# Kernel optimization log

Hardware: AMD Instinct MI355X
Metric: run time of the kernel (lower is better)

## Reference

```python
import jax, jax.numpy as jnp
import numpy as np

B, C_IN, FH, TW = 64, 8, 128, 128
FBINS, A, M_ARR, M_SRC = 257, 360, 4, 2
EPS = 1e-6


def _conv2d(x, w):
    return jax.lax.conv_general_dilated(x, w, (1, 1), 'SAME', dimension_numbers=('NCHW', 'OIHW', 'NCHW'))


def _bn(x, g, b, m, v):
    sh = (1, -1, 1, 1)
    return (x - m.reshape(sh)) * jax.lax.rsqrt(v.reshape(sh) + 1e-5) * g.reshape(sh) + b.reshape(sh)


def _pool2(x):
    b_, c, h, w = x.shape
    return x.reshape(b_, c, h // 2, 2, w // 2, 2).max(axis=(3, 5))


def _block(x, w, g, b, m, v):
    return _pool2(jax.nn.relu(_bn(_conv2d(x, w), g, b, m, v)))


def _conv1d(x, w, b):
    return jax.lax.conv_general_dilated(x, w, (1,), 'SAME', dimension_numbers=('NCH', 'OIH', 'NCH')) + b[None, :, None]


def setup_inputs() -> dict:
    ks = jax.random.split(jax.random.key(0), 16)
    r = lambda i, shp, s=1.0: jax.random.normal(ks[i], shp, dtype=jnp.float32) * s
    d = {
        'X': r(0, (B, C_IN, FH, TW)),
        'sv_real': r(1, (B, FBINS, A, M_ARR)),
        'sv_imag': r(2, (B, FBINS, A, M_ARR)),
        'correlation': jnp.zeros((1,), jnp.float32),
        'conv1_w': r(3, (64, C_IN, 3, 3), 0.1),
        'conv2_w': r(4, (64, 64, 3, 3), 0.04),
        'conv3_w': r(5, (64, 64, 3, 3), 0.04),
        'conv4_w': r(6, (FBINS, 64, 3, 3), 0.04),
        'fc_w': r(7, (32, 64), 0.1),
        'fc_b': jnp.zeros((32,), jnp.float32),
        'convs2_w': r(8, (FBINS, FBINS, 3), 0.02),
        'convs2_b': jnp.zeros((FBINS,), jnp.float32),
        'convs1_w': r(9, (1, FBINS, 3), 0.03),
        'convs1_b': jnp.zeros((1,), jnp.float32),
        'ca_w1': r(10, (16, FBINS), 0.06),
        'ca_w2': r(11, (FBINS, 16), 0.2),
    }
    for i, c in [(1, 64), (2, 64), (3, 64), (4, FBINS)]:
        d[f'bn{i}_g'] = jnp.ones((c,), jnp.float32)
        d[f'bn{i}_b'] = jnp.zeros((c,), jnp.float32)
        d[f'bn{i}_m'] = jnp.zeros((c,), jnp.float32)
        d[f'bn{i}_v'] = jnp.ones((c,), jnp.float32)
    return d


def reference(X, sv_real, sv_imag, correlation,
              conv1_w, bn1_g, bn1_b, bn1_m, bn1_v,
              conv2_w, bn2_g, bn2_b, bn2_m, bn2_v,
              conv3_w, bn3_g, bn3_b, bn3_m, bn3_v,
              conv4_w, bn4_g, bn4_b, bn4_m, bn4_v,
              fc_w, fc_b, convs2_w, convs2_b, convs1_w, convs1_b,
              ca_w1, ca_w2):
    b_ = X.shape[0]
    # CNN encoder: (B,8,128,128) -> (B,257,8,8)
    z = _block(X, conv1_w, bn1_g, bn1_b, bn1_m, bn1_v)
    z = _block(z, conv2_w, bn2_g, bn2_b, bn2_m, bn2_v)
    z = _block(z, conv3_w, bn3_g, bn3_b, bn3_m, bn3_v)
    z = _block(z, conv4_w, bn4_g, bn4_b, bn4_m, bn4_v)
    z = z.reshape(b_, FBINS, -1) @ fc_w.T + fc_b            # (B,257,32)
    z = z.reshape(b_, FBINS, C_IN // 2, C_IN)               # (B,257,4,8)
    Rz = jax.lax.complex(z[..., :M_ARR], z[..., M_ARR:])    # (B,257,4,4)
    # hermitianize + diagonal loading
    Rz = 0.5 * (Rz + jnp.conj(jnp.swapaxes(Rz, -1, -2)))
    Rz = Rz + 1e-5 * jnp.eye(M_ARR, dtype=Rz.dtype)
    _, evecs = jnp.linalg.eigh(Rz)                          # ascending eigenvalues
    Un = evecs[..., ::-1][..., M_SRC:]                      # noise subspace (B,F,4,2)
    UnUnH = Un @ jnp.conj(jnp.swapaxes(Un, -1, -2))         # (B,F,4,4)
    svc = jnp.conj(jax.lax.complex(sv_real, sv_imag))       # (B,F,A,4)
    # faithful to torch code: denom[a] = sum_{m,n} conj(sv[a,m]) UnUnH[m,n] conj(sv[a,n])
    denom = jnp.real(jnp.einsum('bfam,bfmn,bfan->bfa', svc, UnUnH, svc))
    spectrum = 1.0 / jnp.maximum(denom, EPS)                # (B,257,360)
    spectrum = jax.nn.leaky_relu(_conv1d(spectrum, convs2_w, convs2_b), 0.1)
    # channel attention over the 257 freq channels
    y = spectrum.mean(-1)                                   # (B,257)
    att = jax.nn.sigmoid(jax.nn.relu(y @ ca_w1.T) @ ca_w2.T)
    spectrum = spectrum * att[:, :, None]
    spectrum = jax.nn.sigmoid(_conv1d(spectrum, convs1_w, convs1_b))[:, 0, :]  # (B,360)
    # soft-argmax over top-5 peaks
    angles = jnp.linspace(0.0, 360.0, A + 1)[:-1]
    vals, idx = jax.lax.top_k(spectrum, 5)
    wts = jax.nn.softmax(20.0 * vals, axis=-1)
    doa = (wts * angles[idx]).sum(-1)[:, None]              # (B,1)
    return doa, spectrum
```

## Files before the change

kernel.cpp:

```cpp
#include <hip/hip_runtime.h>

typedef unsigned short u16;
typedef unsigned int u32;
typedef short short8 __attribute__((ext_vector_type(8)));
typedef float f32x4 __attribute__((ext_vector_type(4)));

#define NB 64
#define NFB 257
#define NANG 360

template<int V> struct IC { static constexpr int value = V; };

__device__ __forceinline__ u16 f2bf(float x) {
    u32 u = __float_as_uint(x);
    u = (u + 0x7fffu + ((u >> 16) & 1u)) >> 16;
    return (u16)u;
}
__device__ __forceinline__ float bf2f(u16 h) { return __uint_as_float(((u32)h) << 16); }


__global__ __launch_bounds__(256) void bnprep(
    const float* g1, const float* b1, const float* m1, const float* v1,
    const float* g2, const float* b2, const float* m2, const float* v2,
    const float* g3, const float* b3, const float* m3, const float* v3,
    const float* g4, const float* b4, const float* m4, const float* v4,
    float* out)
{
    int L = blockIdx.x;
    const float* gs[4] = {g1, g2, g3, g4};
    const float* bs[4] = {b1, b2, b3, b4};
    const float* ms[4] = {m1, m2, m3, m4};
    const float* vs[4] = {v1, v2, v3, v4};
    int n = (L == 3) ? 257 : 64;
    float* sc = out + L * 1024;
    float* bi = sc + 512;
    for (int i = threadIdx.x; i < n; i += 256) {
        float s = gs[L][i] * rsqrtf(vs[L][i] + 1e-5f);
        sc[i] = s;
        bi[i] = bs[L][i] - ms[L][i] * s;
    }
}

__global__ __launch_bounds__(256) void bpack(
    const float* __restrict__ w, u16* __restrict__ Bp,
    int CREAL, int OCREAL, int NT, int KCC, int NFTOT)
{
    int i = blockIdx.x * 256 + threadIdx.x;
    int total = NT * KCC * 2 * NFTOT * 64;
    if (i >= total) return;
    int lane = i & 63;
    int t = i >> 6;
    int nf = t % NFTOT;
    int th = t / NFTOT;
    int h = th & 1;
    int chunk = th >> 1;
    int s = chunk / KCC, kc = chunk % KCC;
    int n = nf * 16 + (lane & 15);
    int k0 = kc * 32 + (lane >> 4) * 8;
    u16 o8[8];
    #pragma unroll
    for (int e = 0; e < 8; ++e) {
        int k = k0 + e;
        float v = 0.f;
        if (k < CREAL && n < OCREAL) v = w[((size_t)n * CREAL + k) * NT + s];
        u16 hh = f2bf(v);
        o8[e] = (h == 0) ? hh : f2bf(v - bf2f(hh));
    }
    u16* d = Bp + (size_t)i * 8;
    #pragma unroll
    for (int e = 0; e < 8; ++e) d[e] = o8[e];
}

__global__ __launch_bounds__(256) void bpack1(const float* __restrict__ w, u16* __restrict__ Bp)
{
    int i = blockIdx.x * 256 + threadIdx.x;
    if (i >= 3 * 2 * 4 * 64) return;
    int lane = i & 63;
    int t = i >> 6;
    int nf = t % 4;
    int th = t / 4;
    int h = th & 1;
    int ky = th >> 1;
    int n = nf * 16 + (lane & 15);
    int q = lane >> 4;
    u16 o8[8];
    #pragma unroll
    for (int e = 0; e < 8; ++e) {
        float v = (q < 3) ? w[((size_t)(n * 8 + e) * 3 + ky) * 3 + q] : 0.f;
        u16 hh = f2bf(v);
        o8[e] = (h == 0) ? hh : f2bf(v - bf2f(hh));
    }
    u16* d = Bp + (size_t)i * 8;
    #pragma unroll
    for (int e = 0; e < 8; ++e) d[e] = o8[e];
}

__global__ __launch_bounds__(256) void xpack_kernel(
    const float* __restrict__ X, u16* __restrict__ xp)
{
    __shared__ float Xs[8][132];
    int bid = blockIdx.x;
    int prow = bid % 130;
    int b = bid / 130;
    bool inr = (prow >= 1 && prow <= 128);
    for (int i = threadIdx.x; i < 8 * 130; i += 256) {
        int c = i / 130, pcol = i % 130;
        float v = 0.f;
        if (inr && pcol >= 1 && pcol <= 128)
            v = X[(((size_t)b * 8 + c) * 128 + (prow - 1)) * 128 + (pcol - 1)];
        Xs[c][pcol] = v;
    }
    __syncthreads();
    for (int p = threadIdx.x; p < 130; p += 256) {
        short8 h8, l8;
        #pragma unroll
        for (int c = 0; c < 8; ++c) {
            float f = Xs[c][p];
            u16 hh = f2bf(f);
            h8[c] = (short)hh;
            l8[c] = (short)f2bf(f - bf2f(hh));
        }
        size_t o = (((size_t)b * 130 + prow) * 130 + p) * 16;
        *(short8*)(xp + o) = h8;
        *(short8*)(xp + o + 8) = l8;
    }
}

__global__ __launch_bounds__(256) void zpad(
    u32* buf, int Bn, int Hp, int Wp, int wpp, int doCols)
{
    int perB = 2 * Wp + (doCols ? 2 * (Hp - 2) : 0);
    long total = (long)Bn * perB * wpp;
    for (long idx = blockIdx.x * 256L + threadIdx.x; idx < total; idx += (long)gridDim.x * 256) {
        int w = (int)(idx % wpp);
        long t = idx / wpp;
        int p = (int)(t % perB);
        int b = (int)(t / perB);
        int row, col;
        if (p < Wp) { row = 0; col = p; }
        else if (p < 2 * Wp) { row = Hp - 1; col = p - Wp; }
        else { int pp = p - 2 * Wp; row = 1 + (pp >> 1); col = (pp & 1) ? (Wp - 1) : 0; }
        buf[(((size_t)b * Hp + row) * Wp + col) * (size_t)wpp + w] = 0;
    }
}

__global__ __launch_bounds__(256) void conv_c1(
    const u16* __restrict__ A, const u16* __restrict__ Bp,
    const float* __restrict__ esc, const float* __restrict__ ebi,
    u16* __restrict__ O)
{
    constexpr int Wst = 130, Hp = 130;
    constexpr int SROWS = 5;
    constexpr int SPIX = SROWS * Wst;
    __shared__ __align__(16) char sm[SPIX * 48];

    int bid = blockIdx.x;
    int ytile = bid % 64;
    int b = bid / 64;
    int y0 = ytile * 2;
    int tid = threadIdx.x;
    int wv = tid >> 6;
    int l = tid & 63;
    int r = l & 15, q = l >> 4;

    #pragma unroll
    for (int it = 0; it < 3; ++it) {
        int pix = tid + it * 256;
        int prow = y0 + pix / Wst, pcol = pix % Wst;
        uint4 v0 = {0, 0, 0, 0}, v1 = {0, 0, 0, 0};
        if (pix < SPIX && prow < Hp) {
            const u16* src = A + (((size_t)b * Hp + prow) * Wst + pcol) * 16;
            v0 = *(const uint4*)src;
            v1 = *(const uint4*)(src + 8);
        }
        if (pix < SPIX) {
            *(uint4*)(sm + pix * 48) = v0;
            *(uint4*)(sm + pix * 48 + 16) = v1;
        }
    }
    __syncthreads();

    f32x4 acc[4][4] = {};

    #pragma unroll
    for (int ky = 0; ky < 3; ++ky) {
        short8 bh[4], bl[4];
        #pragma unroll
        for (int ni = 0; ni < 4; ++ni) {
            const u16* bt = Bp + ((size_t)(ky * 2) * 4 + ni) * 512 + l * 8;
            bh[ni] = *(const short8*)bt;
            bl[ni] = *(const short8*)(bt + 4 * 512);
        }
        short8 ah[4], al[4];
        #pragma unroll
        for (int mi = 0; mi < 4; ++mi) {
            int pf = wv * 2 + (mi >> 1);
            int y = mi & 1;
            int p = (y + ky) * Wst + pf * 16 + r + q;
            ah[mi] = *(const short8*)(sm + p * 48);
            al[mi] = *(const short8*)(sm + p * 48 + 16);
        }
        #pragma unroll
        for (int ni = 0; ni < 4; ++ni)
            #pragma unroll
            for (int mi = 0; mi < 4; ++mi) {
                acc[mi][ni] = __builtin_amdgcn_mfma_f32_16x16x32_bf16(ah[mi], bh[ni], acc[mi][ni], 0, 0, 0);
                acc[mi][ni] = __builtin_amdgcn_mfma_f32_16x16x32_bf16(ah[mi], bl[ni], acc[mi][ni], 0, 0, 0);
                acc[mi][ni] = __builtin_amdgcn_mfma_f32_16x16x32_bf16(al[mi], bh[ni], acc[mi][ni], 0, 0, 0);
            }
    }

    #pragma unroll
    for (int ni = 0; ni < 4; ++ni) {
        int oc = ni * 16 + r;
        float sc0 = esc[oc], bi0 = ebi[oc];
        #pragma unroll
        for (int pi = 0; pi < 2; ++pi) {
            int pf = wv * 2 + pi;
            #pragma unroll
            for (int k = 0; k < 2; ++k) {
                float m = -3.4e38f;
                #pragma unroll
                for (int dmi = 0; dmi < 2; ++dmi)
                    #pragma unroll
                    for (int dj = 0; dj < 2; ++dj)
                        m = fmaxf(m, fmaf(acc[2 * pi + dmi][ni][2 * k + dj], sc0, bi0));
                m = fmaxf(m, 0.f);
                int x2 = pf * 8 + q * 2 + k;
                size_t base = (((size_t)b * 66 + (y0 / 2 + 1)) * 66 + (x2 + 1)) * 128;
                u16* d = O + base + ((oc >> 5) << 6) + (oc & 31);
                u16 hh = f2bf(m);
                d[0] = hh;
                d[32] = f2bf(m - bf2f(hh));
            }
        }
    }
}

template<int H, int W, int OC, int R, int NF, int MFW, int OUTMODE, int NFTOT>
__global__ __launch_bounds__(256) void conv_gemm(
    const u16* __restrict__ A, const u16* __restrict__ Bp,
    const float* __restrict__ esc, const float* __restrict__ ebi,
    u16* __restrict__ O, float* __restrict__ Of)
{
    constexpr int Wst = W + 2, Hp = H + 2;
    constexpr int SROWS = R + 2;
    constexpr int SPIX = SROWS * Wst;
    constexpr int XF = W / 16;
    constexpr int HT = H / R;
    constexpr int GR = SPIX * 4;
    constexpr int ROUNDS = (GR + 255) / 256;
    __shared__ __align__(16) char sm[SPIX * 128];

    int bid = blockIdx.x;
    int ytile = bid % HT;
    int b = bid / HT;
    int tid = threadIdx.x;
    int wv = tid >> 6;
    int l = tid & 63;
    int r = l & 15, q = l >> 4;
    int y0 = ytile * R;
    int nfg0 = blockIdx.y * NF;

    f32x4 acc[MFW][NF] = {};
    short8 Bh[2][NF], Bl[2][NF];

    auto loadB = [&](int buf, int chunk) {
        #pragma unroll
        for (int ni = 0; ni < NF; ++ni) {
            const u16* bt = Bp + ((size_t)(chunk * 2) * NFTOT + nfg0 + ni) * 512 + l * 8;
            Bh[buf][ni] = *(const short8*)bt;
            Bl[buf][ni] = *(const short8*)(bt + (size_t)NFTOT * 512);
        }
    };

    #pragma unroll
    for (int it = 0; it < ROUNDS; ++it) {
        int idx = tid + it * 256;
        int pix = idx >> 2, sub = idx & 3;
        int prow = y0 + pix / Wst, pcol = pix % Wst;
        uint4 v0 = {0, 0, 0, 0}, v1 = {0, 0, 0, 0};
        if (idx < GR && prow < Hp) {
            const u16* src = A + (((size_t)b * Hp + prow) * Wst + pcol) * 128 + sub * 8;
            v0 = *(const uint4*)src;
            v1 = *(const uint4*)(src + 32);
        }
        if (idx < GR) {
            *(uint4*)(sm + pix * 128 + ((sub ^ (pix & 7)) << 4)) = v0;
            *(uint4*)(sm + pix * 128 + (((sub + 4) ^ (pix & 7)) << 4)) = v1;
        }
    }
    loadB(0, 0);
    __syncthreads();

    auto computePhase = [&](auto csc) {
        constexpr int cs = decltype(csc)::value;
        #pragma unroll
        for (int s = 0; s < 9; ++s) {
            int cur = (cs * 9 + s) & 1;
            if (s < 8) loadB(cur ^ 1, (s + 1) * 2 + cs);
            else if (cs == 0) loadB(cur ^ 1, 1);
            int ky = s / 3, kx = s % 3;
            short8 ah[MFW], al[MFW];
            #pragma unroll
            for (int mi = 0; mi < MFW; ++mi) {
                int pf = wv * (MFW / 2) + (mi >> 1);
                int y = (pf / XF) * 2 + (mi & 1);
                int xf = pf % XF;
                int p = (y + ky) * Wst + xf * 16 + kx + r;
                int off = p * 128 + ((q ^ (p & 7)) << 4);
                ah[mi] = *(const short8*)(sm + off);
                al[mi] = *(const short8*)(sm + (off ^ 64));
            }
            #pragma unroll
            for (int ni = 0; ni < NF; ++ni)
                #pragma unroll
                for (int mi = 0; mi < MFW; ++mi) {
                    acc[mi][ni] = __builtin_amdgcn_mfma_f32_16x16x32_bf16(ah[mi], Bh[cur][ni], acc[mi][ni], 0, 0, 0);
                    acc[mi][ni] = __builtin_amdgcn_mfma_f32_16x16x32_bf16(ah[mi], Bl[cur][ni], acc[mi][ni], 0, 0, 0);
                    acc[mi][ni] = __builtin_amdgcn_mfma_f32_16x16x32_bf16(al[mi], Bh[cur][ni], acc[mi][ni], 0, 0, 0);
                }
        }
    };

    uint4 r0[ROUNDS], r1[ROUNDS];
    #pragma unroll
    for (int it = 0; it < ROUNDS; ++it) {
        int idx = tid + it * 256;
        int pix = idx >> 2, sub = idx & 3;
        int prow = y0 + pix / Wst, pcol = pix % Wst;
        r0[it] = (uint4){0, 0, 0, 0};
        r1[it] = (uint4){0, 0, 0, 0};
        if (idx < GR && prow < Hp) {
            const u16* src = A + (((size_t)b * Hp + prow) * Wst + pcol) * 128 + 64 + sub * 8;
            r0[it] = *(const uint4*)src;
            r1[it] = *(const uint4*)(src + 32);
        }
    }
    computePhase(IC<0>{});
    __syncthreads();
    #pragma unroll
    for (int it = 0; it < ROUNDS; ++it) {
        int idx = tid + it * 256;
        int pix = idx >> 2, sub = idx & 3;
        if (idx < GR) {
            *(uint4*)(sm + pix * 128 + ((sub ^ (pix & 7)) << 4)) = r0[it];
            *(uint4*)(sm + pix * 128 + (((sub + 4) ^ (pix & 7)) << 4)) = r1[it];
        }
    }
    __syncthreads();
    computePhase(IC<1>{});

    #pragma unroll
    for (int ni = 0; ni < NF; ++ni) {
        int oc = (nfg0 + ni) * 16 + r;
        float sc0 = esc[oc], bi0 = ebi[oc];
        #pragma unroll
        for (int pi = 0; pi < MFW / 2; ++pi) {
            int pf = wv * (MFW / 2) + pi;
            int y2 = y0 / 2 + pf / XF;
            int xb = (pf % XF) * 8 + q * 2;
            #pragma unroll
            for (int k = 0; k < 2; ++k) {
                float m = -3.4e38f;
                #pragma unroll
                for (int dmi = 0; dmi < 2; ++dmi)
                    #pragma unroll
                    for (int dj = 0; dj < 2; ++dj)
                        m = fmaxf(m, fmaf(acc[2 * pi + dmi][ni][2 * k + dj], sc0, bi0));
                m = fmaxf(m, 0.f);
                int x2 = xb + k;
                if (OUTMODE == 0) {
                    size_t base = (((size_t)b * (H / 2 + 2) + y2 + 1) * (W / 2 + 2) + (x2 + 1)) * 128;
                    u16* d = O + base + ((oc >> 5) << 6) + (oc & 31);
                    u16 hh = f2bf(m);
                    d[0] = hh;
                    d[32] = f2bf(m - bf2f(hh));
                } else {
                    if (oc < OC)
                        Of[(((size_t)b * (H / 2) + y2) * (W / 2) + x2) * (size_t)OC + oc] = m;
                }
            }
        }
    }
}

__global__ __launch_bounds__(256) void convs2_gemm(
    const u16* __restrict__ A, const u16* __restrict__ Bp,
    const float* __restrict__ bia, float* __restrict__ sp2)
{
    constexpr int SPIX = 194;
    constexpr int GR = SPIX * 4;
    constexpr int ROUNDS = 4;
    __shared__ __align__(16) char sm[SPIX * 128];

    int bid = blockIdx.x;
    int tt = bid & 1;
    int b = bid >> 1;
    int nt = blockIdx.y;
    int t0 = tt * 192;
    int tid = threadIdx.x;
    int wv = tid >> 6;
    int l = tid & 63;
    int r = l & 15, q = l >> 4;

    f32x4 acc[3][3] = {};
    short8 Bh[2][3], Bl[2][3];

    auto loadB = [&](int buf, int chunk) {
        #pragma unroll
        for (int ni = 0; ni < 3; ++ni) {
            const u16* bt = Bp + ((size_t)(chunk * 2) * 18 + nt * 3 + ni) * 512 + l * 8;
            Bh[buf][ni] = *(const short8*)bt;
            Bl[buf][ni] = *(const short8*)(bt + 18 * 512);
        }
    };
    uint4 g0[ROUNDS], g1[ROUNDS];

    auto stageIssue = [&](int cs) {
        #pragma unroll
        for (int it = 0; it < ROUNDS; ++it) {
            int idx = tid + it * 256;
            int pix = idx >> 2, sub = idx & 3;
            int gp = t0 + pix;
            g0[it] = (uint4){0, 0, 0, 0};
            g1[it] = (uint4){0, 0, 0, 0};
            if (idx < GR && gp < 362) {
                const u16* src = A + ((size_t)b * 362 + gp) * 576 + cs * 64 + sub * 8;
                g0[it] = *(const uint4*)src;
                g1[it] = *(const uint4*)(src + 32);
            }
        }
    };
    auto stageWrite = [&]() {
        #pragma unroll
        for (int it = 0; it < ROUNDS; ++it) {
            int idx = tid + it * 256;
            int pix = idx >> 2, sub = idx & 3;
            if (idx < GR) {
                *(uint4*)(sm + pix * 128 + ((sub ^ (pix & 7)) << 4)) = g0[it];
                *(uint4*)(sm + pix * 128 + (((sub + 4) ^ (pix & 7)) << 4)) = g1[it];
            }
        }
    };

    stageIssue(0);
    stageWrite();
    loadB(0, 0);
    __syncthreads();

    #pragma unroll
    for (int cs = 0; cs < 9; ++cs) {
        if (cs < 8) stageIssue(cs + 1);
        #pragma unroll
        for (int ky = 0; ky < 3; ++ky) {
            int cur = (cs * 3 + ky) & 1;
            if (ky < 2) loadB(cur ^ 1, (ky + 1) * 9 + cs);
            else if (cs < 8) loadB(cur ^ 1, cs + 1);
            #pragma unroll
            for (int mi = 0; mi < 3; ++mi) {
                int p = (wv * 3 + mi) * 16 + r + ky;
                int off = p * 128 + ((q ^ (p & 7)) << 4);
                short8 ah = *(const short8*)(sm + off);
                short8 al = *(const short8*)(sm + (off ^ 64));
                #pragma unroll
                for (int ni = 0; ni < 3; ++ni) {
                    acc[mi][ni] = __builtin_amdgcn_mfma_f32_16x16x32_bf16(ah, Bh[cur][ni], acc[mi][ni], 0, 0, 0);
                    acc[mi][ni] = __builtin_amdgcn_mfma_f32_16x16x32_bf16(ah, Bl[cur][ni], acc[mi][ni], 0, 0, 0);
                    acc[mi][ni] = __builtin_amdgcn_mfma_f32_16x16x32_bf16(al, Bh[cur][ni], acc[mi][ni], 0, 0, 0);
                }
            }
        }
        __syncthreads();
        if (cs < 8) {
            stageWrite();
            __syncthreads();
        }
    }

    #pragma unroll
    for (int ni = 0; ni < 3; ++ni) {
        int n = (nt * 3 + ni) * 16 + r;
        if (n >= NFB) continue;
        float bi0 = bia[n];
        #pragma unroll
        for (int mi = 0; mi < 3; ++mi) {
            int tb = t0 + (wv * 3 + mi) * 16 + q * 4;
            #pragma unroll
            for (int j = 0; j < 4; ++j) {
                int t = tb + j;
                if (t < NANG) {
                    float v = acc[mi][ni][j] + bi0;
                    sp2[((size_t)b * NANG + t) * NFB + n] = (v >= 0.f) ? v : 0.1f * v;
                }
            }
        }
    }
}

__global__ __launch_bounds__(256) void fc_kernel(
    const float* __restrict__ z, const float* __restrict__ fw,
    const float* __restrict__ fb, float* __restrict__ zfc)
{
    int bid = blockIdx.x;
    int ftile = bid % 33;
    int b = bid / 33;
    int j = threadIdx.x & 31;
    int f = ftile * 8 + (threadIdx.x >> 5);
    if (f >= 257) return;
    const float* zb = z + (size_t)b * 16448;
    float a = fb[j];
    #pragma unroll 8
    for (int s = 0; s < 64; ++s) a = fmaf(zb[s * 257 + f], fw[j * 64 + s], a);
    zfc[((size_t)b * 257 + f) * 32 + j] = a;
}

__global__ __launch_bounds__(64) void eigh_kernel(const float* __restrict__ z, double* __restrict__ rp)
{
    int idx = blockIdx.x * 64 + threadIdx.x;
    if (idx >= NB * NFB) return;
    const float* zr = z + (size_t)idx * 32;
    double Ar[4][4], Ai[4][4], Vr[4][4], Vi[4][4];
    #pragma unroll
    for (int m = 0; m < 4; ++m)
        #pragma unroll
        for (int n = 0; n < 4; ++n) {
            Ar[m][n] = 0.5 * ((double)zr[m * 8 + n] + (double)zr[n * 8 + m]);
            Ai[m][n] = 0.5 * ((double)zr[m * 8 + n + 4] - (double)zr[n * 8 + m + 4]);
            Vr[m][n] = (m == n) ? 1.0 : 0.0;
            Vi[m][n] = 0.0;
        }
    #pragma unroll
    for (int m = 0; m < 4; ++m) Ar[m][m] += 1e-5;

    for (int sweep = 0; sweep < 8; ++sweep) {
        #pragma unroll
        for (int p = 0; p < 3; ++p)
            #pragma unroll
            for (int qq = p + 1; qq < 4; ++qq) {
                double apr = Ar[p][qq], api = Ai[p][qq];
                double rmod = sqrt(apr * apr + api * api);
                if (rmod < 1e-300) continue;
                double cph = apr / rmod, sph = api / rmod;
                double tau = (Ar[qq][qq] - Ar[p][p]) / (2.0 * rmod);
                double t = (tau >= 0.0) ? (-1.0 / (tau + sqrt(1.0 + tau * tau)))
                                        : (1.0 / (-tau + sqrt(1.0 + tau * tau)));
                double c = 1.0 / sqrt(1.0 + t * t);
                double s = t * c;
                double wr = s * cph, wi = s * sph;
                #pragma unroll
                for (int i = 0; i < 4; ++i) {
                    double xr = Ar[i][p], xi = Ai[i][p];
                    double yr = Ar[i][qq], yi = Ai[i][qq];
                    Ar[i][p] = c * xr + (wr * yr + wi * yi);
                    Ai[i][p] = c * xi + (wr * yi - wi * yr);
                    Ar[i][qq] = c * yr - (wr * xr - wi * xi);
                    Ai[i][qq] = c * yi - (wr * xi + wi * xr);
                }
                #pragma unroll
                for (int i = 0; i < 4; ++i) {
                    double xr = Ar[p][i], xi = Ai[p][i];
                    double yr = Ar[qq][i], yi = Ai[qq][i];
                    Ar[p][i] = c * xr + (wr * yr - wi * yi);
                    Ai[p][i] = c * xi + (wr * yi + wi * yr);
                    Ar[qq][i] = c * yr - (wr * xr + wi * xi);
                    Ai[qq][i] = c * yi - (wr * xi - wi * xr);
                }
                #pragma unroll
                for (int i = 0; i < 4; ++i) {
                    double xr = Vr[i][p], xi = Vi[i][p];
                    double yr = Vr[i][qq], yi = Vi[i][qq];
                    Vr[i][p] = c * xr + (wr * yr + wi * yi);
                    Vi[i][p] = c * xi + (wr * yi - wi * yr);
                    Vr[i][qq] = c * yr - (wr * xr - wi * xi);
                    Vi[i][qq] = c * yi - (wr * xi + wi * xr);
                }
            }
    }
    double ev[4] = {Ar[0][0], Ar[1][1], Ar[2][2], Ar[3][3]};
    int i0 = 0;
    #pragma unroll
    for (int k = 1; k < 4; ++k) if (ev[k] < ev[i0]) i0 = k;
    int i1 = (i0 == 0) ? 1 : 0;
    #pragma unroll
    for (int k = 0; k < 4; ++k) if (k != i0 && ev[k] < ev[i1]) i1 = k;
    double* o = rp + (size_t)idx * 16;
    #pragma unroll
    for (int m = 0; m < 4; ++m)
        #pragma unroll
        for (int n = 0; n < 4; ++n)
            o[m * 4 + n] = Vr[m][i0] * Vr[n][i0] + Vi[m][i0] * Vi[n][i0]
                         + Vr[m][i1] * Vr[n][i1] + Vi[m][i1] * Vi[n][i1];
}

__global__ __launch_bounds__(256) void music_kernel(
    const float4* __restrict__ svr, const float4* __restrict__ svi,
    const double* __restrict__ rp, u16* __restrict__ mu)
{
    __shared__ double P[32][16];
    __shared__ float T[32][33];
    int bid = blockIdx.x;
    int at = bid % 12; bid /= 12;
    int ft = bid % 9;
    int b = bid / 9;
    int f0 = ft * 32, a0 = at * 32;
    int tid = threadIdx.x;
    for (int i = tid; i < 32 * 16; i += 256) {
        int fi = i >> 4, j = i & 15;
        int f = f0 + fi;
        P[fi][j] = (f < 257) ? rp[((size_t)b * 257 + f) * 16 + j] : 0.0;
    }
    __syncthreads();
    int asub = tid & 31, fsub = tid >> 5;
    int a = a0 + asub;
    #pragma unroll
    for (int k2 = 0; k2 < 4; ++k2) {
        int fl = fsub + 8 * k2;
        int f = f0 + fl;
        float val = 0.f;
        if (a < 360 && f < 257) {
            float4 u = svr[((size_t)b * 257 + f) * 360 + a];
            float4 w = svi[((size_t)b * 257 + f) * 360 + a];
            const double* Pf = P[fl];
            double ua[4] = {u.x, u.y, u.z, u.w};
            double wa[4] = {w.x, w.y, w.z, w.w};
            double qa = 0.0, qb = 0.0;
            #pragma unroll
            for (int m = 0; m < 4; ++m)
                #pragma unroll
                for (int n = 0; n < 4; ++n) {
                    double pmn = Pf[m * 4 + n];
                    qa += pmn * ua[m] * ua[n];
                    qb += pmn * wa[m] * wa[n];
                }
            double den = qa - qb;
            val = (float)(1.0 / fmax(den, 1e-6));
        }
        T[asub][fl] = val;
    }
    __syncthreads();
    int sec0 = f0 >> 5;
    #pragma unroll
    for (int p = 0; p < 4; ++p) {
        int row = p * 8 + (tid >> 5);
        int fc = tid & 31;
        int a2 = a0 + row;
        if (a2 < 360) {
            float v = T[row][fc];
            u16* d = mu + ((size_t)b * 362 + a2 + 1) * 576 + (size_t)sec0 * 64 + fc;
            u16 hh = f2bf(v);
            d[0] = hh;
            d[32] = f2bf(v - bf2f(hh));
        }
    }
}

__global__ __launch_bounds__(256) void attn_partial(const float* __restrict__ sp2, float* __restrict__ part)
{
    int bid = blockIdx.x;
    int ch = bid % 6;
    int b = bid / 6;
    int t0 = ch * 60;
    for (int f = threadIdx.x; f < 257; f += 256) {
        float s = 0.f;
        for (int t = 0; t < 60; ++t) s += sp2[((size_t)b * 360 + t0 + t) * 257 + f];
        part[((size_t)b * 6 + ch) * 257 + f] = s;
    }
}

__global__ __launch_bounds__(256) void attn_finish(
    const float* __restrict__ part, const float* __restrict__ w1,
    const float* __restrict__ w2, float* __restrict__ att)
{
    __shared__ float ys[257];
    __shared__ float hs[16];
    int b = blockIdx.x;
    int tid = threadIdx.x;
    for (int f = tid; f < 257; f += 256) {
        float s = 0.f;
        #pragma unroll
        for (int c = 0; c < 6; ++c) s += part[((size_t)b * 6 + c) * 257 + f];
        ys[f] = s * (1.0f / 360.0f);
    }
    __syncthreads();
    if (tid < 16) {
        float h = 0.f;
        for (int c = 0; c < 257; ++c) h = fmaf(ys[c], w1[(size_t)tid * 257 + c], h);
        hs[tid] = fmaxf(h, 0.f);
    }
    __syncthreads();
    for (int o = tid; o < 257; o += 256) {
        float a = 0.f;
        #pragma unroll
        for (int j = 0; j < 16; ++j) a = fmaf(hs[j], w2[(size_t)o * 16 + j], a);
        att[(size_t)b * 257 + o] = 1.0f / (1.0f + expf(-a));
    }
}

__global__ __launch_bounds__(256) void convs1_kernel(
    const float* __restrict__ sp2, const float* __restrict__ att,
    const float* __restrict__ w, const float* __restrict__ bb,
    float* __restrict__ outS)
{
    int bid = blockIdx.x;
    int tt = bid % 90;
    int b = bid / 90;
    int wv = threadIdx.x >> 6, l = threadIdx.x & 63;
    int t = tt * 4 + wv;
    float s = 0.f;
    for (int f = l; f < 257; f += 64) {
        float av = att[(size_t)b * 257 + f];
        float w0 = w[f * 3] * av, w1 = w[f * 3 + 1] * av, w2 = w[f * 3 + 2] * av;
        const float* col = sp2 + (size_t)b * 360 * 257 + f;
        if (t > 0)   s = fmaf(w0, col[(size_t)(t - 1) * 257], s);
        s = fmaf(w1, col[(size_t)t * 257], s);
        if (t < 359) s = fmaf(w2, col[(size_t)(t + 1) * 257], s);
    }
    #pragma unroll
    for (int off = 32; off > 0; off >>= 1) s += __shfl_down(s, off, 64);
    if (l == 0) outS[(size_t)b * 360 + t] = 1.0f / (1.0f + expf(-(s + bb[0])));
}

__global__ __launch_bounds__(64) void doa_kernel(const float* __restrict__ spec, float* __restrict__ doa)
{
    int b = blockIdx.x;
    int l = threadIdx.x;
    const float* s = spec + (size_t)b * NANG;
    float v[6];
    #pragma unroll
    for (int j = 0; j < 6; ++j) {
        int idx = l + 64 * j;
        v[j] = (idx < NANG) ? s[idx] : -3.4e38f;
    }
    float wvv[5]; int wii[5];
    #pragma unroll
    for (int k = 0; k < 5; ++k) {
        float bv = v[0]; int bj = 0;
        #pragma unroll
        for (int j = 1; j < 6; ++j)
            if (v[j] > bv) { bv = v[j]; bj = j; }
        int bi = l + 64 * bj;
        #pragma unroll
        for (int off = 1; off < 64; off <<= 1) {
            float ov = __shfl_xor(bv, off, 64);
            int oi = __shfl_xor(bi, off, 64);
            if (ov > bv || (ov == bv && oi < bi)) { bv = ov; bi = oi; }
        }
        wvv[k] = bv; wii[k] = bi;
        if ((bi & 63) == l) {
            int j = bi >> 6;
            #pragma unroll
            for (int jj = 0; jj < 6; ++jj)
                if (jj == j) v[jj] = -3.4e38f;
        }
    }
    if (l == 0) {
        float m = wvv[0];
        float wsum = 0.f, asum = 0.f;
        #pragma unroll
        for (int k = 0; k < 5; ++k) {
            float e = expf(20.0f * (wvv[k] - m));
            wsum += e;
            asum += e * (float)wii[k];
        }
        doa[b] = asum / wsum;
    }
}

extern "C" void kernel_launch(void* const* d_in, const int* in_sizes, int n_in,
                              void* d_out, int out_size, void* d_ws, size_t ws_size,
                              hipStream_t stream)
{
    const float* X    = (const float*)d_in[0];
    const float* svr  = (const float*)d_in[1];
    const float* svi  = (const float*)d_in[2];
    const float* c1w  = (const float*)d_in[4];
    const float* c2w  = (const float*)d_in[5];
    const float* c3w  = (const float*)d_in[6];
    const float* c4w  = (const float*)d_in[7];
    const float* fcw  = (const float*)d_in[8];
    const float* fcb  = (const float*)d_in[9];
    const float* s2w  = (const float*)d_in[10];
    const float* s2b  = (const float*)d_in[11];
    const float* s1w  = (const float*)d_in[12];
    const float* s1b  = (const float*)d_in[13];
    const float* caw1 = (const float*)d_in[14];
    const float* caw2 = (const float*)d_in[15];
    const float* bn1g = (const float*)d_in[16]; const float* bn1b = (const float*)d_in[17];
    const float* bn1m = (const float*)d_in[18]; const float* bn1v = (const float*)d_in[19];
    const float* bn2g = (const float*)d_in[20]; const float* bn2b = (const float*)d_in[21];
    const float* bn2m = (const float*)d_in[22]; const float* bn2v = (const float*)d_in[23];
    const float* bn3g = (const float*)d_in[24]; const float* bn3b = (const float*)d_in[25];
    const float* bn3m = (const float*)d_in[26]; const float* bn3v = (const float*)d_in[27];
    const float* bn4g = (const float*)d_in[28]; const float* bn4b = (const float*)d_in[29];
    const float* bn4m = (const float*)d_in[30]; const float* bn4v = (const float*)d_in[31];

    char* wsb = (char*)d_ws;
    u16* xp = (u16*)(wsb + 0);
    u16* c3 = (u16*)(wsb + 0);
    u16* mu = (u16*)(wsb + 0);
    const size_t Bb = 34611200;
    u16*   c2  = (u16*)(wsb + Bb);
    float*  zbuf = (float*)(wsb + Bb);
    float*  zfc  = (float*)(wsb + Bb + 4210688);
    double* rp   = (double*)(wsb + Bb + 6316032);
    float*  sp2  = (float*)(wsb + Bb + 8421376);
    float*  part = (float*)(wsb + Bb + 32106496);
    float*  att  = (float*)(wsb + Bb + 32501248);
    const size_t Cb = Bb + 71368704;
    u16* c4  = (u16*)(wsb + Cb);
    u16* bp1 = (u16*)(wsb + Cb + 5308416);
    u16* bp2 = (u16*)(wsb + Cb + 5382144);
    u16* bp3 = (u16*)(wsb + Cb + 5529600);
    u16* bp4 = (u16*)(wsb + Cb + 5677056);
    u16* bp5 = (u16*)(wsb + Cb + 6414336);
    float* bns = (float*)(wsb + Cb + 7409664);

    float* outD = (float*)d_out;
    float* outS = (float*)d_out + 64;

    bnprep<<<4, 256, 0, stream>>>(bn1g, bn1b, bn1m, bn1v, bn2g, bn2b, bn2m, bn2v,
                                  bn3g, bn3b, bn3m, bn3v, bn4g, bn4b, bn4m, bn4v, bns);
    bpack1<<<6, 256, 0, stream>>>(c1w, bp1);
    bpack<<<36, 256, 0, stream>>>(c2w, bp2, 64, 64, 9, 2, 4);
    bpack<<<36, 256, 0, stream>>>(c3w, bp3, 64, 64, 9, 2, 4);
    bpack<<<180, 256, 0, stream>>>(c4w, bp4, 64, 257, 9, 2, 20);
    bpack<<<243, 256, 0, stream>>>(s2w, bp5, 257, 257, 3, 9, 18);
    xpack_kernel<<<64 * 130, 256, 0, stream>>>(X, xp);
    zpad<<<4160, 256, 0, stream>>>((u32*)c2, 64, 66, 66, 64, 1);
    zpad<<<1088, 256, 0, stream>>>((u32*)c4, 64, 18, 18, 64, 1);

    conv_c1<<<64 * 64, 256, 0, stream>>>(xp, bp1, bns, bns + 512, c2);
    zpad<<<2112, 256, 0, stream>>>((u32*)c3, 64, 34, 34, 64, 1);
    conv_gemm<64, 64, 64, 2, 4, 2, 0, 4>
        <<<dim3(64 * 32, 1), 256, 0, stream>>>(c2, bp2, bns + 1024, bns + 1536, c3, nullptr);
    conv_gemm<32, 32, 64, 4, 4, 2, 0, 4>
        <<<dim3(64 * 8, 1), 256, 0, stream>>>(c3, bp3, bns + 2048, bns + 2560, c4, nullptr);
    zpad<<<144, 256, 0, stream>>>((u32*)mu, 64, 362, 1, 288, 0);
    conv_gemm<16, 16, 257, 8, 4, 2, 1, 20>
        <<<dim3(64 * 2, 5), 256, 0, stream>>>(c4, bp4, bns + 3072, bns + 3584, nullptr, zbuf);

    fc_kernel<<<64 * 33, 256, 0, stream>>>(zbuf, fcw, fcb, zfc);
    eigh_kernel<<<NFB, 64, 0, stream>>>(zfc, rp);
    music_kernel<<<64 * 108, 256, 0, stream>>>((const float4*)svr, (const float4*)svi, rp, mu);
    convs2_gemm<<<dim3(64 * 2, 6), 256, 0, stream>>>(mu, bp5, s2b, sp2);

    attn_partial<<<64 * 6, 256, 0, stream>>>(sp2, part);
    attn_finish<<<64, 256, 0, stream>>>(part, caw1, caw2, att);
    convs1_kernel<<<64 * 90, 256, 0, stream>>>(sp2, att, s1w, s1b, outS);
    doa_kernel<<<64, 64, 0, stream>>>(outS, outD);
}
```

Before: 425.3 us.

## Fuse channel-attention mean into convs2 epilogue and regroup MFMA issue order

The per-channel time sums for channel attention are now computed in the convs2 GEMM epilogue with a wave shuffle and shared-memory reduction, written as two partials per batch, and the separate attn_partial kernel is removed. That drops one launch and a full re-read of the spectrum buffer. Separately, the three split-bf16 MFMA passes in all conv kernels are split into three loop nests, so consecutive MFMAs no longer hit the same accumulator back to back. The extra epilogue reduction and sync add a little work to the GEMM.

```diff
diff --git a/kernel.cpp b/kernel.cpp
--- a/kernel.cpp
+++ b/kernel.cpp
@@ -203,11 +203,18 @@
         #pragma unroll
         for (int ni = 0; ni < 4; ++ni)
             #pragma unroll
-            for (int mi = 0; mi < 4; ++mi) {
+            for (int mi = 0; mi < 4; ++mi)
                 acc[mi][ni] = __builtin_amdgcn_mfma_f32_16x16x32_bf16(ah[mi], bh[ni], acc[mi][ni], 0, 0, 0);
+        #pragma unroll
+        for (int ni = 0; ni < 4; ++ni)
+            #pragma unroll
+            for (int mi = 0; mi < 4; ++mi)
                 acc[mi][ni] = __builtin_amdgcn_mfma_f32_16x16x32_bf16(ah[mi], bl[ni], acc[mi][ni], 0, 0, 0);
+        #pragma unroll
+        for (int ni = 0; ni < 4; ++ni)
+            #pragma unroll
+            for (int mi = 0; mi < 4; ++mi)
                 acc[mi][ni] = __builtin_amdgcn_mfma_f32_16x16x32_bf16(al[mi], bh[ni], acc[mi][ni], 0, 0, 0);
-            }
     }
 
     #pragma unroll
@@ -315,11 +322,18 @@
             #pragma unroll
             for (int ni = 0; ni < NF; ++ni)
                 #pragma unroll
-                for (int mi = 0; mi < MFW; ++mi) {
+                for (int mi = 0; mi < MFW; ++mi)
                     acc[mi][ni] = __builtin_amdgcn_mfma_f32_16x16x32_bf16(ah[mi], Bh[cur][ni], acc[mi][ni], 0, 0, 0);
+            #pragma unroll
+            for (int ni = 0; ni < NF; ++ni)
+                #pragma unroll
+                for (int mi = 0; mi < MFW; ++mi)
                     acc[mi][ni] = __builtin_amdgcn_mfma_f32_16x16x32_bf16(ah[mi], Bl[cur][ni], acc[mi][ni], 0, 0, 0);
+            #pragma unroll
+            for (int ni = 0; ni < NF; ++ni)
+                #pragma unroll
+                for (int mi = 0; mi < MFW; ++mi)
                     acc[mi][ni] = __builtin_amdgcn_mfma_f32_16x16x32_bf16(al[mi], Bh[cur][ni], acc[mi][ni], 0, 0, 0);
-                }
         }
     };
 
@@ -387,7 +401,8 @@
 
 __global__ __launch_bounds__(256) void convs2_gemm(
     const u16* __restrict__ A, const u16* __restrict__ Bp,
-    const float* __restrict__ bia, float* __restrict__ sp2)
+    const float* __restrict__ bia, float* __restrict__ sp2,
+    float* __restrict__ part)
 {
     constexpr int SPIX = 194;
     constexpr int GR = SPIX * 4;
@@ -464,11 +479,14 @@
                 short8 ah = *(const short8*)(sm + off);
                 short8 al = *(const short8*)(sm + (off ^ 64));
                 #pragma unroll
-                for (int ni = 0; ni < 3; ++ni) {
+                for (int ni = 0; ni < 3; ++ni)
                     acc[mi][ni] = __builtin_amdgcn_mfma_f32_16x16x32_bf16(ah, Bh[cur][ni], acc[mi][ni], 0, 0, 0);
+                #pragma unroll
+                for (int ni = 0; ni < 3; ++ni)
                     acc[mi][ni] = __builtin_amdgcn_mfma_f32_16x16x32_bf16(ah, Bl[cur][ni], acc[mi][ni], 0, 0, 0);
+                #pragma unroll
+                for (int ni = 0; ni < 3; ++ni)
                     acc[mi][ni] = __builtin_amdgcn_mfma_f32_16x16x32_bf16(al, Bh[cur][ni], acc[mi][ni], 0, 0, 0);
-                }
             }
         }
         __syncthreads();
@@ -478,6 +496,7 @@
         }
     }
 
+    float psum[3] = {0.f, 0.f, 0.f};
     #pragma unroll
     for (int ni = 0; ni < 3; ++ni) {
         int n = (nt * 3 + ni) * 16 + r;
@@ -491,10 +510,28 @@
                 int t = tb + j;
                 if (t < NANG) {
                     float v = acc[mi][ni][j] + bi0;
-                    sp2[((size_t)b * NANG + t) * NFB + n] = (v >= 0.f) ? v : 0.1f * v;
+                    v = (v >= 0.f) ? v : 0.1f * v;
+                    sp2[((size_t)b * NANG + t) * NFB + n] = v;
+                    psum[ni] += v;
                 }
             }
         }
+    }
+    float* wred = (float*)sm;
+    #pragma unroll
+    for (int ni = 0; ni < 3; ++ni) {
+        float s = psum[ni];
+        s += __shfl_down(s, 32, 64);
+        s += __shfl_down(s, 16, 64);
+        if (q == 0) wred[(wv * 3 + ni) * 16 + r] = s;
+    }
+    __syncthreads();
+    if (tid < 48) {
+        int ni = tid / 16, rr = tid % 16;
+        float tot = wred[(0 * 3 + ni) * 16 + rr] + wred[(1 * 3 + ni) * 16 + rr]
+                  + wred[(2 * 3 + ni) * 16 + rr] + wred[(3 * 3 + ni) * 16 + rr];
+        int n = (nt * 3 + ni) * 16 + rr;
+        if (n < NFB) part[((size_t)b * 2 + tt) * NFB + n] = tot;
     }
 }
 
@@ -655,19 +692,6 @@
     }
 }
 
-__global__ __launch_bounds__(256) void attn_partial(const float* __restrict__ sp2, float* __restrict__ part)
-{
-    int bid = blockIdx.x;
-    int ch = bid % 6;
-    int b = bid / 6;
-    int t0 = ch * 60;
-    for (int f = threadIdx.x; f < 257; f += 256) {
-        float s = 0.f;
-        for (int t = 0; t < 60; ++t) s += sp2[((size_t)b * 360 + t0 + t) * 257 + f];
-        part[((size_t)b * 6 + ch) * 257 + f] = s;
-    }
-}
-
 __global__ __launch_bounds__(256) void attn_finish(
     const float* __restrict__ part, const float* __restrict__ w1,
     const float* __restrict__ w2, float* __restrict__ att)
@@ -677,9 +701,7 @@
     int b = blockIdx.x;
     int tid = threadIdx.x;
     for (int f = tid; f < 257; f += 256) {
-        float s = 0.f;
-        #pragma unroll
-        for (int c = 0; c < 6; ++c) s += part[((size_t)b * 6 + c) * 257 + f];
+        float s = part[((size_t)b * 2 + 0) * 257 + f] + part[((size_t)b * 2 + 1) * 257 + f];
         ys[f] = s * (1.0f / 360.0f);
     }
     __syncthreads();
@@ -843,9 +865,8 @@
     fc_kernel<<<64 * 33, 256, 0, stream>>>(zbuf, fcw, fcb, zfc);
     eigh_kernel<<<NFB, 64, 0, stream>>>(zfc, rp);
     music_kernel<<<64 * 108, 256, 0, stream>>>((const float4*)svr, (const float4*)svi, rp, mu);
-    convs2_gemm<<<dim3(64 * 2, 6), 256, 0, stream>>>(mu, bp5, s2b, sp2);
-
-    attn_partial<<<64 * 6, 256, 0, stream>>>(sp2, part);
+    convs2_gemm<<<dim3(64 * 2, 6), 256, 0, stream>>>(mu, bp5, s2b, sp2, part);
+
     attn_finish<<<64, 256, 0, stream>>>(part, caw1, caw2, att);
     convs1_kernel<<<64 * 90, 256, 0, stream>>>(sp2, att, s1w, s1b, outS);
     doa_kernel<<<64, 64, 0, stream>>>(outS, outD);
```

After: 416.5 us. -2.1%, faster.
